# Optimization experiments

Measured on AMD Instinct MI355X. Metric: run time of the kernel, lower is better.

## Reference

```python
import jax, jax.numpy as jnp
import numpy as np

BLOCK = 32            # BigBird block size
WINDOW = 128          # sliding-window width in tokens
GLOBAL_BLOCKS = (1, 3, 5)
HEADS = 16
NEG = -1e9


def setup_inputs() -> dict:
    key = jax.random.key(0)
    ks = jax.random.split(key, 5)
    B, S, D = 2, 4096, 1024

    def lin(k):
        k1, k2 = jax.random.split(k)
        lim = 1.0 / np.sqrt(D)
        W = jax.random.uniform(k1, (D, D), minval=-lim, maxval=lim, dtype=jnp.float32)
        b = jax.random.uniform(k2, (D,), minval=-lim, maxval=lim, dtype=jnp.float32)
        return W, b

    Wq, bq = lin(ks[0])
    Wk, bk = lin(ks[1])
    Wv, bv = lin(ks[2])
    Wo, bo = lin(ks[3])
    x = jax.random.normal(ks[4], (B, S, D), dtype=jnp.float32)
    mask = jnp.ones((B, S), dtype=bool)  # True = token is attendable
    return dict(x=x, mask=mask, Wq=Wq, bq=bq, Wk=Wk, bk=bk, Wv=Wv, bv=bv, Wo=Wo, bo=bo)


def bigbird_attn(q, k, v, mask):
    # q,k,v: [B,H,S,Dh]; mask: [B,S] bool
    B, H, S, Dh = q.shape
    nb = S // BLOCK
    G = len(GLOBAL_BLOCKS)
    scale = 1.0 / jnp.sqrt(jnp.asarray(Dh, q.dtype))

    qb = q.reshape(B, H, nb, BLOCK, Dh)
    kb = k.reshape(B, H, nb, BLOCK, Dh)
    vb = v.reshape(B, H, nb, BLOCK, Dh)
    mb = mask.reshape(B, nb, BLOCK)

    w = WINDOW // (2 * BLOCK)                       # window blocks per side (=2)
    offs = jnp.arange(-w, w + 1)                    # [W]=5 neighbor offsets
    nbr = jnp.arange(nb)[:, None] + offs[None, :]   # [nb,W]
    gidx = jnp.array(GLOBAL_BLOCKS)                 # [G]
    # drop out-of-range neighbors and dedupe global blocks from the window set
    valid = (nbr >= 0) & (nbr < nb) & ~jnp.any(nbr[..., None] == gidx, axis=-1)
    nbr_c = jnp.clip(nbr, 0, nb - 1)

    kw = kb[:, :, nbr_c]                            # [B,H,nb,W,BLOCK,Dh]
    vw = vb[:, :, nbr_c]
    mw = mb[:, nbr_c] & valid[None, :, :, None]     # [B,nb,W,BLOCK]
    kg = kb[:, :, gidx]                             # [B,H,G,BLOCK,Dh]
    vg = vb[:, :, gidx]
    mg = mb[:, gidx]                                # [B,G,BLOCK]

    sw = jnp.einsum('bhnqd,bhnwkd->bhnqwk', qb, kw) * scale   # window scores
    sg = jnp.einsum('bhnqd,bhgkd->bhnqgk', qb, kg) * scale    # global-col scores
    sw = jnp.where(mw[:, None, :, None], sw, NEG)
    sg = jnp.where(mg[:, None, None, None], sg, NEG)

    nw = 2 * w + 1
    s = jnp.concatenate([sw.reshape(B, H, nb, BLOCK, nw * BLOCK),
                         sg.reshape(B, H, nb, BLOCK, G * BLOCK)], axis=-1)
    p = jax.nn.softmax(s, axis=-1)
    pw = p[..., :nw * BLOCK].reshape(B, H, nb, BLOCK, nw, BLOCK)
    pg = p[..., nw * BLOCK:].reshape(B, H, nb, BLOCK, G, BLOCK)
    out = (jnp.einsum('bhnqwk,bhnwkd->bhnqd', pw, vw)
           + jnp.einsum('bhnqgk,bhgkd->bhnqd', pg, vg))       # [B,H,nb,BLOCK,Dh]

    # global query blocks attend densely to the full sequence
    qg = qb[:, :, gidx].reshape(B, H, G * BLOCK, Dh)
    sd = jnp.einsum('bhqd,bhkd->bhqk', qg, k) * scale         # [B,H,G*BLOCK,S]
    sd = jnp.where(mask[:, None, None, :], sd, NEG)
    od = jnp.einsum('bhqk,bhkd->bhqd', jax.nn.softmax(sd, axis=-1), v)
    out = out.at[:, :, gidx].set(od.reshape(B, H, G, BLOCK, Dh))
    return out.reshape(B, H, S, Dh)


def reference(x, mask, Wq, bq, Wk, bk, Wv, bv, Wo, bo):
    B, S, D = x.shape
    H = HEADS
    Dh = D // H

    def proj(W, b):
        return (x @ W.T + b).reshape(B, S, H, Dh).transpose(0, 2, 1, 3)

    q = proj(Wq, bq)
    k = proj(Wk, bk)
    v = proj(Wv, bv)
    o = bigbird_attn(q, k, v, mask)          # [B,H,S,Dh]
    o = o.transpose(0, 2, 1, 3).reshape(B, S, D)
    return o @ Wo.T + bo                      # dropout is identity in eval
```

## Files before the change

### kernel.cpp

```cpp
#include <hip/hip_runtime.h>

typedef unsigned short u16;
typedef unsigned int u32;
typedef unsigned long long u64;
typedef __attribute__((ext_vector_type(4))) float f32x4;
typedef __attribute__((ext_vector_type(8))) short s16x8;

constexpr int S = 4096, D = 1024, H = 16, DH = 64, NB = 128;
constexpr size_t BHSTRIDE = (size_t)S * DH;
constexpr int NSPLIT = 16;
constexpr int PSZ = 32*64 + 64;
constexpr size_t XN = (size_t)8192*1024;
constexpr size_t WN = (size_t)1024*1024;
constexpr int NDENSE = 3*32*NSPLIT;

__device__ __forceinline__ float bf2f(u16 u){ union{u32 i; float f;} x; x.i=((u32)u)<<16; return x.f; }
__device__ __forceinline__ u16 f2bf(float f){ union{float f; u32 i;} x; x.f=f; return (u16)((x.i + 0x7FFFu + ((x.i>>16)&1u))>>16); }
__device__ __forceinline__ void gload_lds16(const void* g, void* l){
    __builtin_amdgcn_global_load_lds((const __attribute__((address_space(1))) u32*)g,
                                     (__attribute__((address_space(3))) u32*)l, 16, 0, 0);
}
__device__ __forceinline__ f32x4 mfma16(s16x8 a, s16x8 b, f32x4 c){
    return __builtin_amdgcn_mfma_f32_16x16x32_bf16(a, b, c, 0, 0, 0);
}
__device__ __forceinline__ s16x8 ld8(const u16* p){ return *(const s16x8*)(const void*)p; }
__device__ __forceinline__ s16x8 cvt8(const float* p){
    const f32x4 a = *(const f32x4*)(const void*)p;
    const f32x4 b = *(const f32x4*)(const void*)(p+4);
    union { s16x8 v; u16 h[8]; } r;
    r.h[0]=f2bf(a[0]); r.h[1]=f2bf(a[1]); r.h[2]=f2bf(a[2]); r.h[3]=f2bf(a[3]);
    r.h[4]=f2bf(b[0]); r.h[5]=f2bf(b[1]); r.h[6]=f2bf(b[2]); r.h[7]=f2bf(b[3]);
    return r.v;
}

__global__ __launch_bounds__(256) void convert_bf16(
    const float* __restrict__ x, const float* __restrict__ wq,
    const float* __restrict__ wk, const float* __restrict__ wv,
    const float* __restrict__ wo,
    u16* __restrict__ xb, u16* __restrict__ wb, u16* __restrict__ wob)
{
    const size_t i8 = ((size_t)blockIdx.x*256 + threadIdx.x) * 8;
    const float* src; u16* dst; size_t off;
    if (i8 < XN)            { src = x;  dst = xb;          off = i8; }
    else if (i8 < XN+WN)    { src = wq; dst = wb;          off = i8 - XN; }
    else if (i8 < XN+2*WN)  { src = wk; dst = wb + WN;     off = i8 - XN - WN; }
    else if (i8 < XN+3*WN)  { src = wv; dst = wb + 2*WN;   off = i8 - XN - 2*WN; }
    else                    { src = wo; dst = wob;         off = i8 - XN - 3*WN; }
    *(s16x8*)(void*)(dst + off) = cvt8(src + off);
}

template<int MODE>
__global__ __launch_bounds__(256) void gemm2p(
    const u16* __restrict__ Asrc, const u16* __restrict__ Bsrc,
    const float* __restrict__ b0, const float* __restrict__ b1, const float* __restrict__ b2,
    u16* oq, u16* ok, u16* ovt, float* ofp)
{
    __shared__ __align__(16) u16 smem[16384];
    const int t = threadIdx.x, lane = t & 63, wave = t >> 6;
    const int fr = lane & 15, fq = lane >> 4;
    const int wr = wave >> 1, wc = wave & 1;
    int mt, nt;
    if (MODE == 0){ const int swz = (blockIdx.x & 7)*192 + (blockIdx.x >> 3); mt = swz/24; nt = swz%24; }
    else          { const int swz = (blockIdx.x & 7)*64  + (blockIdx.x >> 3); mt = swz/8;  nt = swz%8; }
    const int m0 = mt*128, n0 = nt*128;

    const int ra = t >> 2, ca = (t & 3) * 8;

    auto aAddr = [&](int row, int k0)->const u16*{
        if (MODE == 0) return Asrc + (size_t)row*1024 + k0 + ca;
        const int b = row >> 12, s = row & (S-1);
        return Asrc + ((size_t)(b*H + (k0 >> 6))*S + s)*DH + (k0 & 63) + ca;
    };
    auto stage = [&](int buf, int k0){
        u16* As = smem + buf*4096;
        u16* Bs = smem + 8192 + buf*4096;
        gload_lds16(aAddr(m0 + ra, k0),      &As[t*8]);
        gload_lds16(aAddr(m0 + 64 + ra, k0), &As[2048 + t*8]);
        gload_lds16(Bsrc + (size_t)(n0 + ra)*1024 + k0 + ca,      &Bs[t*8]);
        gload_lds16(Bsrc + (size_t)(n0 + 64 + ra)*1024 + k0 + ca, &Bs[2048 + t*8]);
    };

    f32x4 acc[4][4] = {};
    stage(0, 0);
    __syncthreads();
    int buf = 0;
    for (int k0 = 0; k0 < 1024; k0 += 32){
        if (k0 + 32 < 1024) stage(buf^1, k0 + 32);
        __builtin_amdgcn_sched_barrier(0);
        const u16* As = smem + buf*4096;
        const u16* Bs = smem + 8192 + buf*4096;
        s16x8 af[4], bf_[4];
        #pragma unroll
        for (int i=0;i<4;i++) af[i]  = ld8(&As[(wr*64 + i*16 + fr)*32 + fq*8]);
        #pragma unroll
        for (int j=0;j<4;j++) bf_[j] = ld8(&Bs[(wc*64 + j*16 + fr)*32 + fq*8]);
        #pragma unroll
        for (int i=0;i<4;i++)
          #pragma unroll
          for (int j=0;j<4;j++)
            acc[i][j] = mfma16(af[i], bf_[j], acc[i][j]);
        __syncthreads();
        buf ^= 1;
    }

    const int z = (MODE == 0) ? (nt >> 3) : 0;
    const int b = m0 >> 12, h0 = (n0 & 1023) >> 6, sloc = m0 & (S-1);
    #pragma unroll
    for (int hp=0; hp<2; hp++){
        if (hp) __syncthreads();
        if (wr == hp){
            #pragma unroll
            for (int j=0;j<4;j++){
                const int lc = wc*64 + j*16 + fr;
                const int cw = (n0 + lc) & 1023;
                const float bv = (MODE == 0) ? (z==0 ? b0[cw] : (z==1 ? b1[cw] : b2[cw])) : b0[n0 + lc];
                #pragma unroll
                for (int i=0;i<4;i++){
                    const int lr = i*16 + fq*4;
                    if (MODE == 0 && z == 2){
                        union{u16 h[4]; u64 u;} pk;
                        #pragma unroll
                        for (int r=0;r<4;r++) pk.h[r] = f2bf(acc[i][j][r] + bv);
                        *(u64*)(void*)&smem[lc*68 + lr] = pk.u;
                    } else {
                        #pragma unroll
                        for (int r=0;r<4;r++) smem[(lr + r)*136 + lc] = f2bf(acc[i][j][r] + bv);
                    }
                }
            }
        }
        __syncthreads();
        #pragma unroll
        for (int p=0;p<4;p++){
            const int idx = p*256 + t;
            if (MODE == 1){
                const int rr = idx >> 4, cc = (idx & 15)*8;
                const s16x8 v = ld8(&smem[rr*136 + cc]);
                f32x4 lo, hi;
                #pragma unroll
                for (int e=0;e<4;e++){ lo[e] = bf2f((u16)v[e]); hi[e] = bf2f((u16)v[4+e]); }
                float* dst = ofp + (size_t)(m0 + hp*64 + rr)*1024 + n0 + cc;
                *(f32x4*)(void*)dst = lo;
                *(f32x4*)(void*)(dst + 4) = hi;
            } else if (z == 2){
                const int rr = idx >> 3, cc = (idx & 7)*8;
                const s16x8 v = ld8(&smem[rr*68 + cc]);
                u16* dst = ovt + ((size_t)(b*H + h0 + (rr>>6))*DH + (rr & 63))*S + sloc + hp*64 + cc;
                *(s16x8*)(void*)dst = v;
            } else {
                const int rr = idx >> 4, cc = (idx & 15)*8;
                const s16x8 v = ld8(&smem[rr*136 + cc]);
                u16* outk = (z == 0) ? oq : ok;
                u16* dst = outk + ((size_t)(b*H + h0 + (cc>>6))*S + sloc + hp*64 + rr)*DH + (cc & 63);
                *(s16x8*)(void*)dst = v;
            }
        }
    }
}

__global__ __launch_bounds__(512) void attn_fused(
    const u16* q, const u16* __restrict__ k, const u16* __restrict__ vt,
    u16* out, float* part)
{
    __shared__ float Mw[8][32], Lw[8][32], Ltot[32], Gm[32];
    __shared__ __align__(16) char Ubuf[4*32*68*4];
    u16   (*Plds)[32][40] = (u16  (*)[32][40])Ubuf;
    float (*reg4)[32][68] = (float(*)[32][68])Ubuf;

    const int t = threadIdx.x, lane = t & 63, w = t >> 6;
    const int fr = lane & 15, fq = lane >> 4;
    const int bid = blockIdx.x;
    const bool dense = bid < NDENSE;
    int n, bh, gq = 0, spl = 0;
    if (dense){
        const int idx = (bid & 7)*192 + (bid >> 3);
        gq = idx % 3; bh = (idx/3) & 31; spl = idx / 96;
        n = 2*gq + 1;
    } else {
        const int sidx = bid - NDENSE;
        const int idx = (sidx & 7)*500 + (sidx >> 3);
        const int i = idx % 125; bh = idx / 125;
        n = i + (i>=1) + (i>=2) + (i>=3);
    }
    const size_t base = (size_t)bh * BHSTRIDE;
    const u16* qp = q + base + (size_t)n*32*DH;

    int kb; bool valid;
    if (dense)      { kb = spl*8 + w; valid = true; }
    else if (w < 5) { kb = n - 2 + w; valid = (kb>=0) & (kb<NB) & (kb!=1) & (kb!=3) & (kb!=5); }
    else            { kb = (w==5)?1:((w==6)?3:5); valid = true; }

    s16x8 qf[2][2];
    #pragma unroll
    for (int qi=0;qi<2;qi++)
      #pragma unroll
      for (int ks=0;ks<2;ks++)
        qf[qi][ks] = ld8(qp + (qi*16 + fr)*DH + ks*32 + fq*8);

    s16x8 kf[2][2] = {}, vf[4] = {};
    if (valid){
        const u16* kbp = k + base + (size_t)kb*32*DH;
        #pragma unroll
        for (int kt=0;kt<2;kt++)
          #pragma unroll
          for (int ks=0;ks<2;ks++)
            kf[kt][ks] = ld8(kbp + (kt*16 + fr)*DH + ks*32 + fq*8);
        const u16* vp = vt + base;
        #pragma unroll
        for (int di=0;di<4;di++)
            vf[di] = ld8(vp + (size_t)(di*16 + fr)*S + kb*32 + fq*8);
    }

    f32x4 st[2][2];
    #pragma unroll
    for (int kt=0;kt<2;kt++)
      #pragma unroll
      for (int qi=0;qi<2;qi++){
        f32x4 c = {};
        c = mfma16(kf[kt][0], qf[qi][0], c);
        c = mfma16(kf[kt][1], qf[qi][1], c);
        st[kt][qi] = c;
      }

    #pragma unroll
    for (int qi=0;qi<2;qi++){
        float bm = st[0][qi][0];
        #pragma unroll
        for (int r=1;r<4;r++) bm = fmaxf(bm, st[0][qi][r]);
        #pragma unroll
        for (int r=0;r<4;r++) bm = fmaxf(bm, st[1][qi][r]);
        bm = fmaxf(bm, __shfl_xor(bm, 16));
        bm = fmaxf(bm, __shfl_xor(bm, 32));
        bm = valid ? bm * 0.125f : -__builtin_inff();
        if (fq == 0) Mw[w][qi*16 + fr] = bm;
    }
    __syncthreads();

    float gm[2];
    #pragma unroll
    for (int qi=0;qi<2;qi++){
        const int qq = qi*16 + fr;
        float g = Mw[0][qq];
        #pragma unroll
        for (int w2=1;w2<8;w2++) g = fmaxf(g, Mw[w2][qq]);
        gm[qi] = g;
    }
    if (dense && w == 0 && fq == 0){ Gm[fr] = gm[0]; Gm[16 + fr] = gm[1]; }

    float p[2][2][4];
    #pragma unroll
    for (int qi=0;qi<2;qi++){
        float rs = 0.f;
        #pragma unroll
        for (int kt=0;kt<2;kt++)
          #pragma unroll
          for (int r=0;r<4;r++){
            const float e = valid ? __expf(st[kt][qi][r]*0.125f - gm[qi]) : 0.f;
            p[kt][qi][r] = e;
            rs += e;
          }
        rs += __shfl_xor(rs, 16);
        rs += __shfl_xor(rs, 32);
        if (fq == 0) Lw[w][qi*16 + fr] = rs;
    }

    #pragma unroll
    for (int kt=0;kt<2;kt++)
      #pragma unroll
      for (int qi=0;qi<2;qi++){
        union { u16 h[4]; unsigned long long u; } pk;
        #pragma unroll
        for (int r=0;r<4;r++) pk.h[r] = f2bf(p[kt][qi][r]);
        *(unsigned long long*)(void*)&Plds[w][qi*16 + fr][kt*16 + fq*4] = pk.u;
      }
    asm volatile("s_waitcnt lgkmcnt(0)" ::: "memory");
    s16x8 pf[2];
    #pragma unroll
    for (int mi=0;mi<2;mi++) pf[mi] = ld8(&Plds[w][mi*16 + fr][fq*8]);
    f32x4 acc[2][4] = {};
    #pragma unroll
    for (int mi=0;mi<2;mi++)
      #pragma unroll
      for (int di=0;di<4;di++)
        acc[mi][di] = mfma16(pf[mi], vf[di], acc[mi][di]);

    __syncthreads();
    if (t < 32){
        float sl = 0.f;
        #pragma unroll
        for (int w2=0;w2<8;w2++) sl += Lw[w2][t];
        Ltot[t] = sl;
    }

    #define STORE_ACC(RI) { \
        _Pragma("unroll") for (int mi=0;mi<2;mi++) \
        _Pragma("unroll") for (int di=0;di<4;di++) \
        _Pragma("unroll") for (int r=0;r<4;r++) \
            reg4[RI][mi*16 + fq*4 + r][di*16 + fr] = acc[mi][di][r]; }
    #define ADD_ACC(RI) { \
        _Pragma("unroll") for (int mi=0;mi<2;mi++) \
        _Pragma("unroll") for (int di=0;di<4;di++) \
        _Pragma("unroll") for (int r=0;r<4;r++) \
            acc[mi][di][r] += reg4[RI][mi*16 + fq*4 + r][di*16 + fr]; }

    if (w >= 4) STORE_ACC(w - 4);
    __syncthreads();
    if (w < 4) ADD_ACC(w);
    __syncthreads();
    if (w == 2) STORE_ACC(0);
    if (w == 3) STORE_ACC(1);
    __syncthreads();
    if (w == 0) ADD_ACC(0);
    if (w == 1) ADD_ACC(1);
    __syncthreads();
    if (w == 1) STORE_ACC(0);
    __syncthreads();
    if (w == 0){
        ADD_ACC(0);
        if (!dense){
            #pragma unroll
            for (int mi=0;mi<2;mi++)
              #pragma unroll
              for (int r=0;r<4;r++){
                const int qq = mi*16 + fq*4 + r;
                const float inv = 1.f / Ltot[qq];
                #pragma unroll
                for (int di=0;di<4;di++)
                    out[base + ((size_t)n*32 + qq)*DH + di*16 + fr] = f2bf(acc[mi][di][r] * inv);
              }
        } else {
            float* pb = part + (((size_t)gq*32 + bh)*NSPLIT + spl)*PSZ;
            #pragma unroll
            for (int mi=0;mi<2;mi++)
              #pragma unroll
              for (int di=0;di<4;di++)
                #pragma unroll
                for (int r=0;r<4;r++)
                    pb[(mi*16 + fq*4 + r)*64 + di*16 + fr] = acc[mi][di][r];
            if (lane < 32){ pb[2048 + lane] = Gm[lane]; pb[2080 + lane] = Ltot[lane]; }
        }
    }
    #undef STORE_ACC
    #undef ADD_ACC
}

__global__ __launch_bounds__(256) void attn_combine(const float* __restrict__ part, u16* out){
    const int g = blockIdx.x;
    const int gq = g >> 5, bh = g & 31, n = 2*gq + 1;
    const int t = threadIdx.x;
    const int qq = t >> 3, j0 = (t & 7) * 8;
    const float* pb = part + ((size_t)g * NSPLIT) * PSZ;
    float gm = -__builtin_inff();
    #pragma unroll
    for (int s=0;s<NSPLIT;s++) gm = fmaxf(gm, pb[s*PSZ + 2048 + qq]);
    float lt = 0.f, o[8] = {};
    for (int s=0;s<NSPLIT;s++){
        const float* ps = pb + s*PSZ;
        const float f = __expf(ps[2048 + qq] - gm);
        lt += ps[2080 + qq] * f;
        #pragma unroll
        for (int j=0;j<8;j++) o[j] += ps[qq*64 + j0 + j] * f;
    }
    const float inv = 1.f / lt;
    union { u16 h[8]; s16x8 v; } ov;
    #pragma unroll
    for (int j=0;j<8;j++) ov.h[j] = f2bf(o[j] * inv);
    *(s16x8*)(void*)(out + (size_t)bh*BHSTRIDE + ((size_t)n*32 + qq)*DH + j0) = ov.v;
}

extern "C" void kernel_launch(void* const* d_in, const int* in_sizes, int n_in,
                              void* d_out, int out_size, void* d_ws, size_t ws_size,
                              hipStream_t stream){
    const float* x  = (const float*)d_in[0];
    const float* Wq = (const float*)d_in[2]; const float* bq = (const float*)d_in[3];
    const float* Wk = (const float*)d_in[4]; const float* bk = (const float*)d_in[5];
    const float* Wv = (const float*)d_in[6]; const float* bv = (const float*)d_in[7];
    const float* Wo = (const float*)d_in[8]; const float* bo = (const float*)d_in[9];
    float* out = (float*)d_out;

    char* ws = (char*)d_ws;
    constexpr size_t TSZ = (size_t)2*H*S*DH*sizeof(u16);
    u16* qa = (u16*)(ws + 0*TSZ);
    u16* kk = (u16*)(ws + 1*TSZ);
    u16* vt = (u16*)(ws + 2*TSZ);

    u16* xb = (u16*)d_out;
    u16* wb = xb + XN;
    u16* wo_b = wb + 3*WN;
    float* dpart = (float*)d_out;

    convert_bf16<<<6144, 256, 0, stream>>>(x, Wq, Wk, Wv, Wo, xb, wb, wo_b);
    gemm2p<0><<<1536, 256, 0, stream>>>(xb, wb, bq, bk, bv, qa, kk, vt, nullptr);
    attn_fused<<<NDENSE + 4000, 512, 0, stream>>>(qa, kk, vt, qa, dpart);
    attn_combine<<<96, 256, 0, stream>>>(dpart, qa);
    gemm2p<1><<<512, 256, 0, stream>>>(qa, wo_b, bo, bo, bo, nullptr, nullptr, nullptr, out);
}
```

Baseline: 195.0 us.

## Assign one sparse query block per wave with online softmax

Sparse query blocks used to be spread across all 8 waves of a workgroup, one key block per wave, and combined through LDS reductions and barriers. Now each wave handles a whole query block on its own, looping over the 8 key blocks with an online softmax, so no cross-wave reduction or barriers are needed. The sparse grid drops from 4000 workgroups to 500. The XCD-aware block mapping is reworked, and the dense path loses its validity branches. Each wave now runs a serial chain of 8 steps, which exposes more load latency per wave.

```diff
diff --git a/kernel.cpp b/kernel.cpp
--- a/kernel.cpp
+++ b/kernel.cpp
@@ -13,6 +13,7 @@
 constexpr size_t XN = (size_t)8192*1024;
 constexpr size_t WN = (size_t)1024*1024;
 constexpr int NDENSE = 3*32*NSPLIT;
+constexpr int NSPARSE_BLK = 500;
 
 __device__ __forceinline__ float bf2f(u16 u){ union{u32 i; float f;} x; x.i=((u32)u)<<16; return x.f; }
 __device__ __forceinline__ u16 f2bf(float f){ union{float f; u32 i;} x; x.f=f; return (u16)((x.i + 0x7FFFu + ((x.i>>16)&1u))>>16); }
@@ -170,25 +171,136 @@
     const int t = threadIdx.x, lane = t & 63, w = t >> 6;
     const int fr = lane & 15, fq = lane >> 4;
     const int bid = blockIdx.x;
-    const bool dense = bid < NDENSE;
-    int n, bh, gq = 0, spl = 0;
-    if (dense){
-        const int idx = (bid & 7)*192 + (bid >> 3);
-        gq = idx % 3; bh = (idx/3) & 31; spl = idx / 96;
-        n = 2*gq + 1;
-    } else {
+
+    if (bid >= NDENSE){
         const int sidx = bid - NDENSE;
-        const int idx = (sidx & 7)*500 + (sidx >> 3);
-        const int i = idx % 125; bh = idx / 125;
-        n = i + (i>=1) + (i>=2) + (i>=3);
-    }
+        const int xcd = sidx & 7, off = sidx >> 3;
+        const int q8 = NSPARSE_BLK/8, r8 = NSPARSE_BLK%8;
+        const int rblk = (xcd < r8 ? xcd*(q8+1) : r8*(q8+1) + (xcd-r8)*q8) + off;
+        const int g = rblk*8 + w;
+        const int i = g % 125, bh = g / 125;
+        const int n = i + (i>=1) + (i>=2) + (i>=3);
+        const size_t base = (size_t)bh * BHSTRIDE;
+        const u16* qp = q  + base + (size_t)n*32*DH;
+        const u16* kp = k  + base;
+        const u16* vp = vt + base;
+
+        s16x8 qf[2][2];
+        #pragma unroll
+        for (int qi=0;qi<2;qi++)
+          #pragma unroll
+          for (int ks=0;ks<2;ks++)
+            qf[qi][ks] = ld8(qp + (qi*16 + fr)*DH + ks*32 + fq*8);
+
+        f32x4 acc[2][4] = {};
+        float mrow[2] = {-__builtin_inff(), -__builtin_inff()};
+        float lrow[2] = {0.f, 0.f};
+
+        #pragma unroll
+        for (int s = 0; s < 8; ++s){
+            int kb; bool valid;
+            if (s < 5){ kb = n - 2 + s; valid = (kb>=0) & (kb<NB) & (kb!=1) & (kb!=3) & (kb!=5); }
+            else      { kb = (s==5)?1:((s==6)?3:5); valid = true; }
+            if (!valid) continue;
+
+            const u16* kbp = kp + (size_t)kb*32*DH;
+            s16x8 kf[2][2], vf[4];
+            #pragma unroll
+            for (int kt=0;kt<2;kt++)
+              #pragma unroll
+              for (int ks=0;ks<2;ks++)
+                kf[kt][ks] = ld8(kbp + (kt*16 + fr)*DH + ks*32 + fq*8);
+            #pragma unroll
+            for (int di=0;di<4;di++)
+                vf[di] = ld8(vp + (size_t)(di*16 + fr)*S + kb*32 + fq*8);
+
+            f32x4 st[2][2];
+            #pragma unroll
+            for (int kt=0;kt<2;kt++)
+              #pragma unroll
+              for (int qi=0;qi<2;qi++){
+                f32x4 c = {};
+                c = mfma16(kf[kt][0], qf[qi][0], c);
+                c = mfma16(kf[kt][1], qf[qi][1], c);
+                st[kt][qi] = c;
+              }
+
+            float fac[2], p[2][2][4];
+            #pragma unroll
+            for (int qi=0;qi<2;qi++){
+                float bm = st[0][qi][0];
+                #pragma unroll
+                for (int r=1;r<4;r++) bm = fmaxf(bm, st[0][qi][r]);
+                #pragma unroll
+                for (int r=0;r<4;r++) bm = fmaxf(bm, st[1][qi][r]);
+                bm = fmaxf(bm, __shfl_xor(bm, 16));
+                bm = fmaxf(bm, __shfl_xor(bm, 32));
+                const float mn = fmaxf(mrow[qi], bm * 0.125f);
+                fac[qi] = __expf(mrow[qi] - mn);
+                float rs = 0.f;
+                #pragma unroll
+                for (int kt=0;kt<2;kt++)
+                  #pragma unroll
+                  for (int r=0;r<4;r++){
+                    const float e = __expf(st[kt][qi][r]*0.125f - mn);
+                    p[kt][qi][r] = e;
+                    rs += e;
+                  }
+                rs += __shfl_xor(rs, 16);
+                rs += __shfl_xor(rs, 32);
+                lrow[qi] = lrow[qi]*fac[qi] + rs;
+                mrow[qi] = mn;
+            }
+            #pragma unroll
+            for (int mi=0;mi<2;mi++){
+                float fa[4];
+                #pragma unroll
+                for (int r=0;r<4;r++) fa[r] = __shfl(fac[mi], fq*4 + r);
+                #pragma unroll
+                for (int di=0;di<4;di++)
+                  #pragma unroll
+                  for (int r=0;r<4;r++)
+                    acc[mi][di][r] *= fa[r];
+            }
+            #pragma unroll
+            for (int kt=0;kt<2;kt++)
+              #pragma unroll
+              for (int qi=0;qi<2;qi++){
+                union { u16 h[4]; u64 u; } pk;
+                #pragma unroll
+                for (int r=0;r<4;r++) pk.h[r] = f2bf(p[kt][qi][r]);
+                *(u64*)(void*)&Plds[w][qi*16 + fr][kt*16 + fq*4] = pk.u;
+              }
+            asm volatile("s_waitcnt lgkmcnt(0)" ::: "memory");
+            s16x8 pf[2];
+            #pragma unroll
+            for (int mi=0;mi<2;mi++) pf[mi] = ld8(&Plds[w][mi*16 + fr][fq*8]);
+            #pragma unroll
+            for (int mi=0;mi<2;mi++)
+              #pragma unroll
+              for (int di=0;di<4;di++)
+                acc[mi][di] = mfma16(pf[mi], vf[di], acc[mi][di]);
+        }
+
+        #pragma unroll
+        for (int mi=0;mi<2;mi++)
+          #pragma unroll
+          for (int r=0;r<4;r++){
+            const int rr = fq*4 + r;
+            const float linv = 1.f / __shfl(lrow[mi], rr);
+            #pragma unroll
+            for (int di=0;di<4;di++)
+                out[base + ((size_t)n*32 + mi*16 + rr)*DH + di*16 + fr] = f2bf(acc[mi][di][r] * linv);
+          }
+        return;
+    }
+
+    const int idx = (bid & 7)*192 + (bid >> 3);
+    const int gq = idx % 3, bh = (idx/3) & 31, spl = idx / 96;
+    const int n = 2*gq + 1;
     const size_t base = (size_t)bh * BHSTRIDE;
     const u16* qp = q + base + (size_t)n*32*DH;
-
-    int kb; bool valid;
-    if (dense)      { kb = spl*8 + w; valid = true; }
-    else if (w < 5) { kb = n - 2 + w; valid = (kb>=0) & (kb<NB) & (kb!=1) & (kb!=3) & (kb!=5); }
-    else            { kb = (w==5)?1:((w==6)?3:5); valid = true; }
+    const int kb = spl*8 + w;
 
     s16x8 qf[2][2];
     #pragma unroll
@@ -197,8 +309,8 @@
       for (int ks=0;ks<2;ks++)
         qf[qi][ks] = ld8(qp + (qi*16 + fr)*DH + ks*32 + fq*8);
 
-    s16x8 kf[2][2] = {}, vf[4] = {};
-    if (valid){
+    s16x8 kf[2][2], vf[4];
+    {
         const u16* kbp = k + base + (size_t)kb*32*DH;
         #pragma unroll
         for (int kt=0;kt<2;kt++)
@@ -231,7 +343,7 @@
         for (int r=0;r<4;r++) bm = fmaxf(bm, st[1][qi][r]);
         bm = fmaxf(bm, __shfl_xor(bm, 16));
         bm = fmaxf(bm, __shfl_xor(bm, 32));
-        bm = valid ? bm * 0.125f : -__builtin_inff();
+        bm = bm * 0.125f;
         if (fq == 0) Mw[w][qi*16 + fr] = bm;
     }
     __syncthreads();
@@ -245,7 +357,7 @@
         for (int w2=1;w2<8;w2++) g = fmaxf(g, Mw[w2][qq]);
         gm[qi] = g;
     }
-    if (dense && w == 0 && fq == 0){ Gm[fr] = gm[0]; Gm[16 + fr] = gm[1]; }
+    if (w == 0 && fq == 0){ Gm[fr] = gm[0]; Gm[16 + fr] = gm[1]; }
 
     float p[2][2][4];
     #pragma unroll
@@ -255,7 +367,7 @@
         for (int kt=0;kt<2;kt++)
           #pragma unroll
           for (int r=0;r<4;r++){
-            const float e = valid ? __expf(st[kt][qi][r]*0.125f - gm[qi]) : 0.f;
+            const float e = __expf(st[kt][qi][r]*0.125f - gm[qi]);
             p[kt][qi][r] = e;
             rs += e;
           }
@@ -268,10 +380,10 @@
     for (int kt=0;kt<2;kt++)
       #pragma unroll
       for (int qi=0;qi<2;qi++){
-        union { u16 h[4]; unsigned long long u; } pk;
+        union { u16 h[4]; u64 u; } pk;
         #pragma unroll
         for (int r=0;r<4;r++) pk.h[r] = f2bf(p[kt][qi][r]);
-        *(unsigned long long*)(void*)&Plds[w][qi*16 + fr][kt*16 + fq*4] = pk.u;
+        *(u64*)(void*)&Plds[w][qi*16 + fr][kt*16 + fq*4] = pk.u;
       }
     asm volatile("s_waitcnt lgkmcnt(0)" ::: "memory");
     s16x8 pf[2];
@@ -317,28 +429,15 @@
     __syncthreads();
     if (w == 0){
         ADD_ACC(0);
-        if (!dense){
-            #pragma unroll
-            for (int mi=0;mi<2;mi++)
-              #pragma unroll
-              for (int r=0;r<4;r++){
-                const int qq = mi*16 + fq*4 + r;
-                const float inv = 1.f / Ltot[qq];
-                #pragma unroll
-                for (int di=0;di<4;di++)
-                    out[base + ((size_t)n*32 + qq)*DH + di*16 + fr] = f2bf(acc[mi][di][r] * inv);
-              }
-        } else {
-            float* pb = part + (((size_t)gq*32 + bh)*NSPLIT + spl)*PSZ;
-            #pragma unroll
-            for (int mi=0;mi<2;mi++)
-              #pragma unroll
-              for (int di=0;di<4;di++)
-                #pragma unroll
-                for (int r=0;r<4;r++)
-                    pb[(mi*16 + fq*4 + r)*64 + di*16 + fr] = acc[mi][di][r];
-            if (lane < 32){ pb[2048 + lane] = Gm[lane]; pb[2080 + lane] = Ltot[lane]; }
-        }
+        float* pb = part + (((size_t)gq*32 + bh)*NSPLIT + spl)*PSZ;
+        #pragma unroll
+        for (int mi=0;mi<2;mi++)
+          #pragma unroll
+          for (int di=0;di<4;di++)
+            #pragma unroll
+            for (int r=0;r<4;r++)
+                pb[(mi*16 + fq*4 + r)*64 + di*16 + fr] = acc[mi][di][r];
+        if (lane < 32){ pb[2048 + lane] = Gm[lane]; pb[2080 + lane] = Ltot[lane]; }
     }
     #undef STORE_ACC
     #undef ADD_ACC
@@ -391,7 +490,7 @@
 
     convert_bf16<<<6144, 256, 0, stream>>>(x, Wq, Wk, Wv, Wo, xb, wb, wo_b);
     gemm2p<0><<<1536, 256, 0, stream>>>(xb, wb, bq, bk, bv, qa, kk, vt, nullptr);
-    attn_fused<<<NDENSE + 4000, 512, 0, stream>>>(qa, kk, vt, qa, dpart);
+    attn_fused<<<NDENSE + NSPARSE_BLK, 512, 0, stream>>>(qa, kk, vt, qa, dpart);
     attn_combine<<<96, 256, 0, stream>>>(dpart, qa);
     gemm2p<1><<<512, 256, 0, stream>>>(qa, wo_b, bo, bo, bo, nullptr, nullptr, nullptr, out);
 }
```

After: 173.6 us. -11.0%, faster.
